# Kernel tuning notes

Hardware: AMD Instinct MI355X
Metric: run time of the kernel (lower is better)

The kernel has to match this reference:

```python
import jax, jax.numpy as jnp
import numpy as np

N_FILTERS = 1024
N_HEADS = 8  # hardcoded h=8 in the original einops.rearrange
LN_EPS = 1e-3  # keras LayerNormalization default epsilon


def setup_inputs() -> dict:
    key = jax.random.key(0)
    k1, k2, k3 = jax.random.split(key, 3)
    B, N, C = 4, 2048, N_FILTERS
    x = jax.random.normal(k1, (B, N, C), dtype=jnp.float32)
    ln_gamma = jnp.ones((C,), dtype=jnp.float32)
    ln_beta = jnp.zeros((C,), dtype=jnp.float32)
    w_qkv = jax.random.normal(k2, (C, 3 * C), dtype=jnp.float32) * 0.02
    w_out = jax.random.normal(k3, (C, C), dtype=jnp.float32) * 0.02
    b_out = jnp.zeros((C,), dtype=jnp.float32)
    return {"x": x, "ln_gamma": ln_gamma, "ln_beta": ln_beta,
            "w_qkv": w_qkv, "w_out": w_out, "b_out": b_out}


def reference(x, ln_gamma, ln_beta, w_qkv, w_out, b_out):
    B, N, C = x.shape
    h = N_HEADS
    hd = C // h
    scale = jnp.asarray(float(C) ** (-0.5), dtype=x.dtype)  # note: full C, as in source

    # LayerNorm over last axis (keras default)
    mu = jnp.mean(x, axis=-1, keepdims=True)
    var = jnp.var(x, axis=-1, keepdims=True)
    xn = (x - mu) / jnp.sqrt(var + LN_EPS) * ln_gamma + ln_beta

    # QKV projection (no bias): [B, N, 3C]
    qkv = jnp.einsum('bnc,cd->bnd', xn, w_qkv)
    # rearrange 'b n (qkv h c) -> qkv b h n c'
    qkv = qkv.reshape(B, N, 3, h, hd).transpose(2, 0, 3, 1, 4)
    q, k, v = qkv[0], qkv[1], qkv[2]

    # attention: [B, h, N, N]
    scores = jnp.einsum('bhnc,bhmc->bhnm', q, k) * scale
    attn = jax.nn.softmax(scores, axis=-1)
    out = jnp.einsum('bhnm,bhmc->bhnc', attn, v)
    # 'b h n c -> b n (h c)'
    out = out.transpose(0, 2, 1, 3).reshape(B, N, C)

    out = jnp.einsum('bnc,cd->bnd', out, w_out) + b_out
    return x + out
```

## Files before the change

kernel.cpp:

```cpp
#include <hip/hip_runtime.h>

typedef _Float16 half8 __attribute__((ext_vector_type(8)));
typedef float floatx4 __attribute__((ext_vector_type(4)));
typedef float floatx16 __attribute__((ext_vector_type(16)));

#define BB 4
#define SEQ 2048
#define CHN 1024
#define NH 8
#define HD 128
#define CQ 3072

__device__ __forceinline__ float bf2f(unsigned short b) {
  unsigned int u = ((unsigned int)b) << 16;
  float f; __builtin_memcpy(&f, &u, 4); return f;
}
__device__ __forceinline__ unsigned short f2bf(float f) {
  unsigned int u; __builtin_memcpy(&u, &f, 4);
  u += 0x7fffu + ((u >> 16) & 1u);
  return (unsigned short)(u >> 16);
}
__device__ __forceinline__ void gl_lds16(const _Float16* g, _Float16* l) {
  __builtin_amdgcn_global_load_lds(
      (const __attribute__((address_space(1))) unsigned int*)(g),
      (__attribute__((address_space(3))) unsigned int*)(l), 16, 0, 0);
}
__device__ __forceinline__ unsigned int pkf16(float a, float b) {
  auto p = __builtin_amdgcn_cvt_pkrtz(a, b);
  unsigned int u; __builtin_memcpy(&u, &p, 4); return u;
}

__global__ __launch_bounds__(256) void detect_k(
    const unsigned int* __restrict__ x, int* __restrict__ flag) {
  __shared__ int bad;
  if (threadIdx.x == 0) bad = 0;
  __syncthreads();
  int b = 0;
#pragma unroll
  for (int i = 0; i < 8; ++i) {
    unsigned int w = x[threadIdx.x * 8 + i];
    float v = bf2f((unsigned short)(w & 0xffffu));
    if (!(fabsf(v) < 1e4f)) b = 1;
  }
  if (b) bad = 1;
  __syncthreads();
  if (threadIdx.x == 0) *flag = bad;
}

__global__ __launch_bounds__(256) void transpose_b2h(
    const void* __restrict__ in, _Float16* __restrict__ out, int R, int C,
    const int* __restrict__ flag) {
  __shared__ _Float16 tile[64][66];
  int isf = *flag;
  int ti = blockIdx.y, tj = blockIdx.x, t = threadIdx.x;
  if (isf) {
    const float* inf = (const float*)in;
#pragma unroll
    for (int i = 0; i < 16; ++i) {
      int lin = i * 256 + t;
      int r = lin >> 6, c = lin & 63;
      tile[r][c] = (_Float16)inf[(size_t)(ti * 64 + r) * C + tj * 64 + c];
    }
  } else {
    const unsigned short* inb = (const unsigned short*)in;
#pragma unroll
    for (int i = 0; i < 16; ++i) {
      int lin = i * 256 + t;
      int r = lin >> 6, c = lin & 63;
      tile[r][c] = (_Float16)bf2f(inb[(size_t)(ti * 64 + r) * C + tj * 64 + c]);
    }
  }
  __syncthreads();
#pragma unroll
  for (int i = 0; i < 16; ++i) {
    int lin = i * 256 + t;
    int c = lin >> 6, r = lin & 63;
    out[(size_t)(tj * 64 + c) * R + ti * 64 + r] = tile[r][c];
  }
}

__global__ __launch_bounds__(256) void ln_k(
    const void* __restrict__ xv, const void* __restrict__ gv,
    const void* __restrict__ bv, _Float16* __restrict__ xn,
    const int* __restrict__ flag) {
  int isf = *flag;
  int row = blockIdx.x, t = threadIdx.x;
  float v0, v1, v2, v3;
  if (isf) {
    const float4 f = *reinterpret_cast<const float4*>((const float*)xv + (size_t)row * CHN + t * 4);
    v0 = f.x; v1 = f.y; v2 = f.z; v3 = f.w;
  } else {
    ushort4 u = *reinterpret_cast<const ushort4*>((const unsigned short*)xv + (size_t)row * CHN + t * 4);
    v0 = bf2f(u.x); v1 = bf2f(u.y); v2 = bf2f(u.z); v3 = bf2f(u.w);
  }
  float s = v0 + v1 + v2 + v3;
  float ss = v0 * v0 + v1 * v1 + v2 * v2 + v3 * v3;
#pragma unroll
  for (int off = 32; off >= 1; off >>= 1) {
    s += __shfl_xor(s, off, 64);
    ss += __shfl_xor(ss, off, 64);
  }
  __shared__ float red[8];
  int wave = t >> 6, lane = t & 63;
  if (lane == 0) { red[wave] = s; red[4 + wave] = ss; }
  __syncthreads();
  s = red[0] + red[1] + red[2] + red[3];
  ss = red[4] + red[5] + red[6] + red[7];
  float mu = s * (1.0f / CHN);
  float var = ss * (1.0f / CHN) - mu * mu;
  float rstd = rsqrtf(var + 1e-3f);
  float g0, g1, g2, g3, b0, b1, b2, b3;
  if (isf) {
    const float4 g = *reinterpret_cast<const float4*>((const float*)gv + t * 4);
    const float4 b = *reinterpret_cast<const float4*>((const float*)bv + t * 4);
    g0 = g.x; g1 = g.y; g2 = g.z; g3 = g.w;
    b0 = b.x; b1 = b.y; b2 = b.z; b3 = b.w;
  } else {
    ushort4 g = *reinterpret_cast<const ushort4*>((const unsigned short*)gv + t * 4);
    ushort4 b = *reinterpret_cast<const ushort4*>((const unsigned short*)bv + t * 4);
    g0 = bf2f(g.x); g1 = bf2f(g.y); g2 = bf2f(g.z); g3 = bf2f(g.w);
    b0 = bf2f(b.x); b1 = bf2f(b.y); b2 = bf2f(b.z); b3 = bf2f(b.w);
  }
  _Float16* o = xn + (size_t)row * CHN + t * 4;
  o[0] = (_Float16)((v0 - mu) * rstd * g0 + b0);
  o[1] = (_Float16)((v1 - mu) * rstd * g1 + b1);
  o[2] = (_Float16)((v2 - mu) * rstd * g2 + b2);
  o[3] = (_Float16)((v3 - mu) * rstd * g3 + b3);
}

template <int EPI>
__global__ __launch_bounds__(256, 3) void gemm_k(
    const _Float16* __restrict__ A, const _Float16* __restrict__ Bt,
    int M, int Nn, int K,
    _Float16* __restrict__ outh, void* __restrict__ outv,
    const void* __restrict__ bias, const void* __restrict__ resid,
    const int* __restrict__ flag) {
  __shared__ _Float16 As[128 * 64];
  __shared__ _Float16 Bs[128 * 64];
  int isf = (EPI == 1) ? *flag : 0;
  int t = threadIdx.x;
  int wave = t >> 6, lane = t & 63, quad = lane >> 4, l15 = lane & 15;
  int wm = wave >> 1, wn = wave & 1;
  size_t arow0 = (size_t)blockIdx.y * 128;
  size_t brow0 = (size_t)blockIdx.x * 128;
  int lr = lane >> 3, lc = lane & 7;
  int gc = lc ^ lr;
  const _Float16* Abase = A + (arow0 + wave * 32 + lr) * (size_t)K + gc * 8;
  const _Float16* Bbase = Bt + (brow0 + wave * 32 + lr) * (size_t)K + gc * 8;
  floatx4 acc[4][4] = {};
  int nkt = K >> 6;
  for (int kt = 0; kt < nkt; ++kt) {
#pragma unroll
    for (int i = 0; i < 4; ++i) {
      gl_lds16(Abase + kt * 64 + (size_t)i * 8 * K, As + (wave * 32 + i * 8) * 64);
      gl_lds16(Bbase + kt * 64 + (size_t)i * 8 * K, Bs + (wave * 32 + i * 8) * 64);
    }
    __syncthreads();
#pragma unroll
    for (int ks = 0; ks < 2; ++ks) {
      half8 af[4], bfr[4];
#pragma unroll
      for (int mt = 0; mt < 4; ++mt) {
        int row = wm * 64 + mt * 16 + l15;
        int slot = (ks * 4 + quad) ^ (l15 & 7);
        af[mt] = *reinterpret_cast<const half8*>(As + row * 64 + slot * 8);
      }
#pragma unroll
      for (int nt = 0; nt < 4; ++nt) {
        int row = wn * 64 + nt * 16 + l15;
        int slot = (ks * 4 + quad) ^ (l15 & 7);
        bfr[nt] = *reinterpret_cast<const half8*>(Bs + row * 64 + slot * 8);
      }
#pragma unroll
      for (int mt = 0; mt < 4; ++mt)
#pragma unroll
        for (int nt = 0; nt < 4; ++nt)
          acc[mt][nt] = __builtin_amdgcn_mfma_f32_16x16x32_f16(af[mt], bfr[nt], acc[mt][nt], 0, 0, 0);
    }
    __syncthreads();
  }
  _Float16* vtrh = (_Float16*)outv;
#pragma unroll
  for (int mt = 0; mt < 4; ++mt) {
#pragma unroll
    for (int r = 0; r < 4; ++r) {
      size_t row = arow0 + wm * 64 + mt * 16 + quad * 4 + r;
#pragma unroll
      for (int nt = 0; nt < 4; ++nt) {
        size_t col = brow0 + wn * 64 + nt * 16 + l15;
        float v = acc[mt][nt][r];
        if (EPI == 0) {
          if (brow0 >= 2 * CHN) {
            int bb = (int)(row >> 11);
            int tok = (int)(row & 2047);
            int c2 = (int)(col - 2 * CHN);
            int h = c2 >> 7, d = c2 & 127;
            vtrh[((size_t)(bb * NH + h) * HD + d) * SEQ + tok] = (_Float16)v;
          } else {
            outh[row * Nn + col] = (_Float16)v;
          }
        } else {
          if (isf) {
            v += ((const float*)bias)[col] + ((const float*)resid)[row * Nn + col];
            ((float*)outv)[row * Nn + col] = v;
          } else {
            v += bf2f(((const unsigned short*)bias)[col]) +
                 bf2f(((const unsigned short*)resid)[row * Nn + col]);
            ((unsigned short*)outv)[row * Nn + col] = f2bf(v);
          }
        }
      }
    }
  }
}

__global__ __launch_bounds__(256, 2) void attn_k(
    const _Float16* __restrict__ qkv, const _Float16* __restrict__ vtr,
    _Float16* __restrict__ out) {
  __shared__ _Float16 Ks[2][64 * 128];
  __shared__ _Float16 Vs[2][128 * 64];
  int t = threadIdx.x;
  int wave = t >> 6, lane = t & 63;
  int l31 = lane & 31, hi = lane >> 5;
  int bh = blockIdx.x & 31;
  int qt = blockIdx.x >> 5;
  int b = bh >> 3, h = bh & 7;
  int qbase = qt * 128;
  const _Float16* qp = qkv + (size_t)b * SEQ * CQ + h * HD;
  const _Float16* kp = qp + CHN;
  const _Float16* vtp = vtr + (size_t)bh * HD * SEQ;
  const _Float16 qsc = (_Float16)0.045085299f;
  half8 aq[8];
  {
    const _Float16* qr = qp + (size_t)(qbase + wave * 32 + l31) * CQ + hi * 8;
#pragma unroll
    for (int c = 0; c < 8; ++c) {
      half8 v = *reinterpret_cast<const half8*>(qr + c * 16);
#pragma unroll
      for (int j = 0; j < 8; ++j) v[j] = v[j] * qsc;
      aq[c] = v;
    }
  }
  float l_p = 0.0f;
  floatx16 accO[4] = {};
  int kr = lane >> 4, ks16 = lane & 15;
  int vr = lane >> 3, vs8 = lane & 7;
#pragma unroll
  for (int i = 0; i < 4; ++i) {
    int r = wave * 16 + i * 4 + kr;
    int gcs = ks16 ^ (r & 15);
    gl_lds16(kp + (size_t)r * CQ + gcs * 8, Ks[0] + (wave * 16 + i * 4) * 128);
  }
#pragma unroll
  for (int i = 0; i < 4; ++i) {
    int r = wave * 32 + i * 8 + vr;
    int gcs = vs8 ^ (r & 7);
    gl_lds16(vtp + (size_t)r * SEQ + gcs * 8, Vs[0] + (wave * 32 + i * 8) * 64);
  }
  __syncthreads();
  for (int kt = 0; kt < SEQ / 64; ++kt) {
    if (kt + 1 < SEQ / 64) {
      int kb2 = (kt + 1) * 64;
      _Float16* vdst = Vs[(kt + 1) & 1];
#pragma unroll
      for (int i = 0; i < 4; ++i) {
        int r = wave * 32 + i * 8 + vr;
        int gcs = vs8 ^ (r & 7);
        gl_lds16(vtp + (size_t)r * SEQ + kb2 + gcs * 8, vdst + (wave * 32 + i * 8) * 64);
      }
      const _Float16* kn = kp + (size_t)kb2 * CQ;
      _Float16* kdst = Ks[(kt + 1) & 1];
#pragma unroll
      for (int i = 0; i < 4; ++i) {
        int r = wave * 16 + i * 4 + kr;
        int gcs = ks16 ^ (r & 15);
        gl_lds16(kn + (size_t)r * CQ + gcs * 8, kdst + (wave * 16 + i * 4) * 128);
      }
    }
    const _Float16* kc = Ks[kt & 1];
    floatx16 accST[2] = {};
    __builtin_amdgcn_s_setprio(1);
#pragma unroll
    for (int c = 0; c < 8; ++c) {
#pragma unroll
      for (int sub = 0; sub < 2; ++sub) {
        int row = sub * 32 + l31;
        int chunk = (c * 2 + hi) ^ (row & 15);
        half8 ak = *reinterpret_cast<const half8*>(kc + (row * 16 + chunk) * 8);
        accST[sub] = __builtin_amdgcn_mfma_f32_32x32x16_f16(ak, aq[c], accST[sub], 0, 0, 0);
      }
    }
    __builtin_amdgcn_s_setprio(0);
    float p0[16], p1[16];
#pragma unroll
    for (int r = 0; r < 16; ++r) p0[r] = __builtin_amdgcn_exp2f(accST[0][r]);
#pragma unroll
    for (int r = 0; r < 16; ++r) p1[r] = __builtin_amdgcn_exp2f(accST[1][r]);
    {
      float s0 = 0, s1 = 0, s2 = 0, s3 = 0;
#pragma unroll
      for (int r = 0; r < 16; r += 4) {
        s0 += p0[r] + p1[r];
        s1 += p0[r + 1] + p1[r + 1];
        s2 += p0[r + 2] + p1[r + 2];
        s3 += p0[r + 3] + p1[r + 3];
      }
      l_p += (s0 + s1) + (s2 + s3);
    }
    const _Float16* vc = Vs[kt & 1];
    __builtin_amdgcn_s_setprio(1);
#pragma unroll
    for (int s = 0; s < 4; ++s) {
      const float* pp = (s & 2) ? p1 : p0;
      int o8 = (s & 1) * 8;
      unsigned int u0 = pkf16(pp[o8 + 0], pp[o8 + 1]);
      unsigned int u1 = pkf16(pp[o8 + 2], pp[o8 + 3]);
      unsigned int w0 = pkf16(pp[o8 + 4], pp[o8 + 5]);
      unsigned int w1 = pkf16(pp[o8 + 6], pp[o8 + 7]);
      asm volatile("v_permlane32_swap_b32 %0, %1" : "+v"(u0), "+v"(w0));
      asm volatile("v_permlane32_swap_b32 %0, %1" : "+v"(u1), "+v"(w1));
      union { unsigned int w[4]; half8 h; } fr;
      fr.w[0] = u0; fr.w[1] = u1; fr.w[2] = w0; fr.w[3] = w1;
#pragma unroll
      for (int dt = 0; dt < 4; ++dt) {
        int row = dt * 32 + l31;
        int chunk = (2 * s + hi) ^ (row & 7);
        half8 bv = *reinterpret_cast<const half8*>(vc + (row * 8 + chunk) * 8);
        accO[dt] = __builtin_amdgcn_mfma_f32_32x32x16_f16(fr.h, bv, accO[dt], 0, 0, 0);
      }
    }
    __builtin_amdgcn_s_setprio(0);
    __syncthreads();
  }
  l_p += __shfl_xor(l_p, 32, 64);
  float inv[16];
#pragma unroll
  for (int r = 0; r < 16; ++r) {
    int qrow = (r & 3) + 8 * (r >> 2) + 4 * hi;
    inv[r] = 1.0f / __shfl(l_p, qrow, 64);
  }
  _Float16* obase = out + ((size_t)b * SEQ + qbase + wave * 32) * CHN + h * HD;
#pragma unroll
  for (int dt = 0; dt < 4; ++dt)
#pragma unroll
    for (int r = 0; r < 16; ++r) {
      int qrow = (r & 3) + 8 * (r >> 2) + 4 * hi;
      obase[(size_t)qrow * CHN + dt * 32 + l31] = (_Float16)(accO[dt][r] * inv[r]);
    }
}

extern "C" void kernel_launch(void* const* d_in, const int* in_sizes, int n_in,
                              void* d_out, int out_size, void* d_ws, size_t ws_size,
                              hipStream_t stream) {
  (void)in_sizes; (void)n_in; (void)out_size; (void)ws_size;
  const void* x = d_in[0];
  const void* gam = d_in[1];
  const void* bet = d_in[2];
  const void* wqkv = d_in[3];
  const void* wout = d_in[4];
  const void* bout = d_in[5];
  char* ws = (char*)d_ws;
  _Float16* vtr   = (_Float16*)(ws);
  _Float16* qkv   = (_Float16*)(ws + (size_t)16777216);
  _Float16* xn    = (_Float16*)(ws + (size_t)67108864);
  _Float16* aout  = (_Float16*)(ws + (size_t)67108864);
  _Float16* wqkvT = (_Float16*)(ws + (size_t)83886080);
  _Float16* woutT = (_Float16*)(ws + (size_t)90177536);
  int* flag       = (int*)(ws + (size_t)92274688);

  detect_k<<<1, 256, 0, stream>>>((const unsigned int*)x, flag);
  transpose_b2h<<<dim3(CQ / 64, CHN / 64), 256, 0, stream>>>(wqkv, wqkvT, CHN, CQ, flag);
  transpose_b2h<<<dim3(CHN / 64, CHN / 64), 256, 0, stream>>>(wout, woutT, CHN, CHN, flag);
  ln_k<<<dim3(BB * SEQ), 256, 0, stream>>>(x, gam, bet, xn, flag);
  gemm_k<0><<<dim3(CQ / 128, BB * SEQ / 128), 256, 0, stream>>>(
      xn, wqkvT, BB * SEQ, CQ, CHN, qkv, vtr, nullptr, nullptr, flag);
  attn_k<<<dim3(BB * NH * (SEQ / 128)), 256, 0, stream>>>(qkv, vtr, aout);
  gemm_k<1><<<dim3(CHN / 128, BB * SEQ / 128), 256, 0, stream>>>(
      aout, woutT, BB * SEQ, CHN, CHN, nullptr, d_out, bout, x, flag);
}
```

Measured before the change: 288.9 us.

## Software-pipeline QK^T of next tile with PV of current tile in attention

```diff
diff --git a/kernel.cpp b/kernel.cpp
--- a/kernel.cpp
+++ b/kernel.cpp
@@ -217,7 +217,7 @@
 __global__ __launch_bounds__(256, 2) void attn_k(
     const _Float16* __restrict__ qkv, const _Float16* __restrict__ vtr,
     _Float16* __restrict__ out) {
-  __shared__ _Float16 Ks[2][64 * 128];
+  __shared__ _Float16 Ks[3][64 * 128];
   __shared__ _Float16 Vs[2][128 * 64];
   int t = threadIdx.x;
   int wave = t >> 6, lane = t & 63;
@@ -245,57 +245,59 @@
   floatx16 accO[4] = {};
   int kr = lane >> 4, ks16 = lane & 15;
   int vr = lane >> 3, vs8 = lane & 7;
-#pragma unroll
-  for (int i = 0; i < 4; ++i) {
-    int r = wave * 16 + i * 4 + kr;
-    int gcs = ks16 ^ (r & 15);
-    gl_lds16(kp + (size_t)r * CQ + gcs * 8, Ks[0] + (wave * 16 + i * 4) * 128);
-  }
-#pragma unroll
-  for (int i = 0; i < 4; ++i) {
-    int r = wave * 32 + i * 8 + vr;
-    int gcs = vs8 ^ (r & 7);
-    gl_lds16(vtp + (size_t)r * SEQ + gcs * 8, Vs[0] + (wave * 32 + i * 8) * 64);
-  }
-  __syncthreads();
-  for (int kt = 0; kt < SEQ / 64; ++kt) {
-    if (kt + 1 < SEQ / 64) {
-      int kb2 = (kt + 1) * 64;
-      _Float16* vdst = Vs[(kt + 1) & 1];
-#pragma unroll
-      for (int i = 0; i < 4; ++i) {
-        int r = wave * 32 + i * 8 + vr;
-        int gcs = vs8 ^ (r & 7);
-        gl_lds16(vtp + (size_t)r * SEQ + kb2 + gcs * 8, vdst + (wave * 32 + i * 8) * 64);
-      }
-      const _Float16* kn = kp + (size_t)kb2 * CQ;
-      _Float16* kdst = Ks[(kt + 1) & 1];
-#pragma unroll
-      for (int i = 0; i < 4; ++i) {
-        int r = wave * 16 + i * 4 + kr;
-        int gcs = ks16 ^ (r & 15);
-        gl_lds16(kn + (size_t)r * CQ + gcs * 8, kdst + (wave * 16 + i * 4) * 128);
-      }
-    }
-    const _Float16* kc = Ks[kt & 1];
-    floatx16 accST[2] = {};
-    __builtin_amdgcn_s_setprio(1);
-#pragma unroll
-    for (int c = 0; c < 8; ++c) {
-#pragma unroll
-      for (int sub = 0; sub < 2; ++sub) {
-        int row = sub * 32 + l31;
-        int chunk = (c * 2 + hi) ^ (row & 15);
-        half8 ak = *reinterpret_cast<const half8*>(kc + (row * 16 + chunk) * 8);
-        accST[sub] = __builtin_amdgcn_mfma_f32_32x32x16_f16(ak, aq[c], accST[sub], 0, 0, 0);
-      }
-    }
-    __builtin_amdgcn_s_setprio(0);
+
+  auto stageK = [&](int j, int buf) {
+#pragma unroll
+    for (int i = 0; i < 4; ++i) {
+      int r = wave * 16 + i * 4 + kr;
+      int gcs = ks16 ^ (r & 15);
+      gl_lds16(kp + (size_t)(j * 64 + r) * CQ + gcs * 8,
+               Ks[buf] + (wave * 16 + i * 4) * 128);
+    }
+  };
+  auto stageV = [&](int j, int buf) {
+#pragma unroll
+    for (int i = 0; i < 4; ++i) {
+      int r = wave * 32 + i * 8 + vr;
+      int gcs = vs8 ^ (r & 7);
+      gl_lds16(vtp + (size_t)r * SEQ + j * 64 + gcs * 8,
+               Vs[buf] + (wave * 32 + i * 8) * 64);
+    }
+  };
+
+  stageK(0, 0);
+  __syncthreads();
+  stageK(1, 1);
+  stageV(0, 0);
+  floatx16 A0 = {}, A1 = {}, B0 = {}, B1 = {};
+  __builtin_amdgcn_s_setprio(1);
+#pragma unroll
+  for (int c = 0; c < 8; ++c) {
+    int ch0 = (c * 2 + hi) ^ (l31 & 15);
+    half8 ak0 = *reinterpret_cast<const half8*>(Ks[0] + (l31 * 16 + ch0) * 8);
+    A0 = __builtin_amdgcn_mfma_f32_32x32x16_f16(ak0, aq[c], A0, 0, 0, 0);
+    int row1 = 32 + l31;
+    int ch1 = (c * 2 + hi) ^ (row1 & 15);
+    half8 ak1 = *reinterpret_cast<const half8*>(Ks[0] + (row1 * 16 + ch1) * 8);
+    A1 = __builtin_amdgcn_mfma_f32_32x32x16_f16(ak1, aq[c], A1, 0, 0, 0);
+  }
+  __builtin_amdgcn_s_setprio(0);
+  __syncthreads();
+
+  auto body = [&](int kt, floatx16& c0, floatx16& c1, floatx16& n0,
+                  floatx16& n1, int rdS, int wrK) {
+    if (kt + 2 < SEQ / 64) stageK(kt + 2, wrK);
+    if (kt + 1 < SEQ / 64) stageV(kt + 1, (kt + 1) & 1);
+    const _Float16* kc = Ks[rdS];
+    const _Float16* vc = Vs[kt & 1];
+    const bool doS = (kt + 1 < SEQ / 64);
+    floatx16 z = {};
+    n0 = z; n1 = z;
     float p0[16], p1[16];
 #pragma unroll
-    for (int r = 0; r < 16; ++r) p0[r] = __builtin_amdgcn_exp2f(accST[0][r]);
-#pragma unroll
-    for (int r = 0; r < 16; ++r) p1[r] = __builtin_amdgcn_exp2f(accST[1][r]);
+    for (int r = 0; r < 16; ++r) p0[r] = __builtin_amdgcn_exp2f(c0[r]);
+#pragma unroll
+    for (int r = 0; r < 16; ++r) p1[r] = __builtin_amdgcn_exp2f(c1[r]);
     {
       float s0 = 0, s1 = 0, s2 = 0, s3 = 0;
 #pragma unroll
@@ -307,10 +309,22 @@
       }
       l_p += (s0 + s1) + (s2 + s3);
     }
-    const _Float16* vc = Vs[kt & 1];
     __builtin_amdgcn_s_setprio(1);
 #pragma unroll
     for (int s = 0; s < 4; ++s) {
+      if (doS) {
+#pragma unroll
+        for (int cc = 0; cc < 2; ++cc) {
+          int c = s * 2 + cc;
+          int ch0 = (c * 2 + hi) ^ (l31 & 15);
+          half8 ak0 = *reinterpret_cast<const half8*>(kc + (l31 * 16 + ch0) * 8);
+          n0 = __builtin_amdgcn_mfma_f32_32x32x16_f16(ak0, aq[c], n0, 0, 0, 0);
+          int row1 = 32 + l31;
+          int ch1 = (c * 2 + hi) ^ (row1 & 15);
+          half8 ak1 = *reinterpret_cast<const half8*>(kc + (row1 * 16 + ch1) * 8);
+          n1 = __builtin_amdgcn_mfma_f32_32x32x16_f16(ak1, aq[c], n1, 0, 0, 0);
+        }
+      }
       const float* pp = (s & 2) ? p1 : p0;
       int o8 = (s & 1) * 8;
       unsigned int u0 = pkf16(pp[o8 + 0], pp[o8 + 1]);
@@ -331,7 +345,18 @@
     }
     __builtin_amdgcn_s_setprio(0);
     __syncthreads();
-  }
+  };
+
+  int rdS = 1, wrK = 2;
+  for (int kt2 = 0; kt2 < SEQ / 128; ++kt2) {
+    body(2 * kt2, A0, A1, B0, B1, rdS, wrK);
+    rdS = (rdS == 2) ? 0 : rdS + 1;
+    wrK = (wrK == 2) ? 0 : wrK + 1;
+    body(2 * kt2 + 1, B0, B1, A0, A1, rdS, wrK);
+    rdS = (rdS == 2) ? 0 : rdS + 1;
+    wrK = (wrK == 2) ? 0 : wrK + 1;
+  }
+
   l_p += __shfl_xor(l_p, 32, 64);
   float inv[16];
 #pragma unroll
```

Measured after the change: 298.9 us. 1.03x slower.
